# Kernel tuning notes

Measured on AMD Instinct MI355X. Metric: run time of the kernel, lower is better.

## Reference

```python
import jax, jax.numpy as jnp
import numpy as np

B, T, N, D, H = 64, 100, 1000, 128, 8
DK = D // H
TANH_CLIP = 10.0  # standard attention-model logit clipping


def setup_inputs() -> dict:
    key = jax.random.key(0)
    ks = jax.random.split(key, 7)
    embeddings = jax.random.normal(ks[0], (B, N, D), jnp.float32)
    Wkvl = jax.random.normal(ks[1], (D, 3 * D), jnp.float32) * 0.05   # project_node_embeddings
    Wfixed = jax.random.normal(ks[2], (D, D), jnp.float32) * 0.05     # project_fixed_context
    Wctx = jax.random.normal(ks[3], (D, D), jnp.float32) * 0.05       # env context projection
    Wout = jax.random.normal(ks[4], (D, D), jnp.float32) * 0.05       # glimpse output projection
    idx = jax.random.randint(ks[5], (T, B), 0, N, jnp.int32)          # current node per decode step
    action_mask = jax.random.uniform(ks[6], (T, B, N)) > 0.2          # True = feasible
    action_mask = action_mask.at[..., 0].set(True)                    # >=1 feasible action per row
    return {"embeddings": embeddings, "Wkvl": Wkvl, "Wfixed": Wfixed,
            "Wctx": Wctx, "Wout": Wout, "idx": idx, "action_mask": action_mask}


def reference(embeddings, Wkvl, Wfixed, Wctx, Wout, idx, action_mask):
    # ---- _precompute ----
    graph_ctx = embeddings.mean(axis=1) @ Wfixed                      # [B, D]
    gk, gv, lk = jnp.split(embeddings @ Wkvl, 3, axis=-1)             # each [B, N, D]

    # ---- all T decode steps batched (dynamic embeddings are zero / static env) ----
    # NOTE: the source overwrites glimpse_key with glimpse_val (glimpse_key = cached.glimpse_val + dyn)
    # and calls logit_attention(query, glimpse_key, glimpse_key, ...), so keys == values == gv.
    cur = jnp.take_along_axis(embeddings, idx.T[..., None], axis=1)   # [B, T, D] current node embed
    query = graph_ctx[:, None, :] + cur @ Wctx                        # [B, T, D]

    q = query.reshape(B, T, H, DK).transpose(0, 2, 1, 3)              # [B, H, T, dk]
    k = gv.reshape(B, N, H, DK).transpose(0, 2, 1, 3)                 # [B, H, N, dk]
    v = k                                                             # keys == values per source

    infeasible = ~action_mask.transpose(1, 0, 2)                      # [B, T, N]

    # glimpse (inner) attention, masked
    compat = jnp.einsum('bhtd,bhnd->bhtn', q, k) / jnp.sqrt(jnp.float32(DK))
    compat = jnp.where(infeasible[:, None], -jnp.inf, compat)
    attn = jax.nn.softmax(compat, axis=-1)                            # [B, H, T, N]
    glimpse = jnp.einsum('bhtn,bhnd->bthd', attn, v).reshape(B, T, D) @ Wout  # [B, T, D]

    # pointer logits with tanh clipping
    logits = jnp.einsum('btd,bnd->btn', glimpse, lk) / jnp.sqrt(jnp.float32(D))
    logits = TANH_CLIP * jnp.tanh(logits)
    logits = jnp.where(infeasible, -jnp.inf, logits)
    return jax.nn.log_softmax(logits, axis=-1)                        # [B, T, N]
```

## Files before the change

kernel.cpp:

```cpp
#include <hip/hip_runtime.h>
#include <math.h>

#define B_  64
#define T_  100
#define N_  1000
#define NP_ 1024
#define TP_ 112
#define D_  128
#define H_  8
#define DK_ 16

#define NEG_BIG (-1e30f)

#define OFF_GVH  0
#define OFF_LKH  16777216
#define OFF_GVT  33554432
#define OFF_CTX  50331648
#define OFF_QH   50364416
#define OFF_GPH  52199424
#define OFF_WT   53837824
#define OFF_WV   53870592
#define OFF_WCT  53936128
#define OFF_PART 53968896
#define OFF_PM   54231040
#define OFF_OPT  55148544
#define OFF_LP   62488576

typedef __attribute__((ext_vector_type(8))) short short8;
typedef __attribute__((ext_vector_type(4))) short bs4;
typedef __attribute__((ext_vector_type(4))) float f32x4;

#if __has_builtin(__builtin_amdgcn_mfma_f32_16x16x16bf16_1k)
#define MFMA16(a, b, c) __builtin_amdgcn_mfma_f32_16x16x16bf16_1k(a, b, c, 0, 0, 0)
#else
__device__ __forceinline__ f32x4 mfma16_asm(bs4 a, bs4 b, f32x4 c) {
    f32x4 d;
    asm volatile("v_mfma_f32_16x16x16_bf16 %0, %1, %2, %3"
                 : "=v"(d) : "v"(a), "v"(b), "v"(c));
    return d;
}
#define MFMA16(a, b, c) mfma16_asm(a, b, c)
#endif

__device__ __forceinline__ unsigned int f2bf(float f) {
    unsigned int u = __float_as_uint(f);
    return (u + 0x7fffu + ((u >> 16) & 1u)) >> 16;
}
__device__ __forceinline__ unsigned int packbf(float a, float b) {
    return f2bf(a) | (f2bf(b) << 16);
}
__device__ __forceinline__ float bf2f(unsigned short u) {
    return __uint_as_float(((unsigned int)u) << 16);
}

__global__ __launch_bounds__(256) void pre_kernel(
        const float* __restrict__ Wkvl, const float* __restrict__ Wout,
        const float* __restrict__ Wctx, const float* __restrict__ emb,
        const unsigned char* __restrict__ am,
        unsigned short* __restrict__ wv, unsigned short* __restrict__ wt,
        unsigned short* __restrict__ wct, float* __restrict__ part,
        unsigned long long* __restrict__ pm) {
    __shared__ float p2[256];
    int bx = blockIdx.x;
    int tid = threadIdx.x;
    if (bx < 256) {
        int i = bx * 256 + tid;
        if (i < 32768) {
            int n = i >> 7, k = i & 127;
            wv[i] = (unsigned short)f2bf(Wkvl[k * 384 + 128 + n]);
        } else if (i < 49152) {
            int j = i - 32768;
            wt[j] = (unsigned short)f2bf(Wout[(j & 127) * D_ + (j >> 7)]);
        } else {
            int j = i - 49152;
            wct[j] = (unsigned short)f2bf(Wctx[(j & 127) * D_ + (j >> 7)]);
        }
    } else if (bx < 768) {
        int b2 = bx - 256;
        int b = b2 >> 3, c = b2 & 7;
        int d = tid & 127, half = tid >> 7;
        int nstart = c * 125 + (half ? 63 : 0);
        int ncnt = half ? 62 : 63;
        const float* e = emb + ((size_t)b * N_ + nstart) * D_ + d;
        float s = 0.f;
        for (int n = 0; n < ncnt; ++n) s += e[(size_t)n * D_];
        p2[tid] = s;
        __syncthreads();
        if (half == 0) part[((size_t)b * 8 + c) * D_ + d] = p2[d] + p2[d + 128];
    } else {
        int rid = bx - 768;
        int t = rid >> 6;
        int wvx = tid >> 6, lane = tid & 63;
        const unsigned char* amrow = am + (size_t)rid * N_;
        unsigned long long* pmrow = pm + (size_t)rid * 16;
        #pragma unroll
        for (int i = 0; i < 4; ++i) {
            int c = wvx * 4 + i;
            int n = c * 64 + lane;
            unsigned char v = (t < T_ && n < N_) ? amrow[n] : (unsigned char)0;
            unsigned long long mb = __ballot(v != 0);
            if (lane == 0) pmrow[c] = mb;
        }
    }
}

__global__ __launch_bounds__(128) void ctxb_kernel(
        const float* __restrict__ part, const float* __restrict__ Wfixed,
        float* __restrict__ ctx) {
    __shared__ float mean[D_];
    int b = blockIdx.x;
    int d = threadIdx.x;
    float s = 0.f;
    for (int c = 0; c < 8; ++c) s += part[((size_t)b * 8 + c) * D_ + d];
    mean[d] = s * (1.0f / N_);
    __syncthreads();
    float acc = 0.f;
    for (int k = 0; k < D_; ++k) acc += mean[k] * Wfixed[k * D_ + d];
    ctx[b * D_ + d] = acc;
}

__global__ __launch_bounds__(256) void proj_kernel(
        const float* __restrict__ emb, const unsigned short* __restrict__ wv,
        unsigned short* __restrict__ gvh, unsigned short* __restrict__ lkh,
        unsigned short* __restrict__ gvT) {
    __shared__ unsigned short As[64 * 136];
    __shared__ unsigned short Gs[64 * 130];
    int rb = blockIdx.x;
    int tid = threadIdx.x;
    int w = tid >> 6, lane = tid & 63, col = lane & 15, quad = lane >> 4;
    const float* a0 = emb + (size_t)rb * 64 * D_;
    #pragma unroll
    for (int i = 0; i < 8; ++i) {
        int idx = tid + i * 256;
        int r = idx >> 5, kq = idx & 31;
        float4 f = *(const float4*)(a0 + r * D_ + kq * 4);
        *(uint2*)&As[r * 136 + kq * 4] = make_uint2(packbf(f.x, f.y), packbf(f.z, f.w));
    }
    __syncthreads();
    short8 bfr[4][4];
    #pragma unroll
    for (int i = 0; i < 4; ++i) {
        int ncol = i * 64 + w * 16 + col;
        #pragma unroll
        for (int kq = 0; kq < 4; ++kq)
            bfr[i][kq] = *(const short8*)(wv + (size_t)ncol * D_ + kq * 32 + quad * 8);
    }
    #pragma unroll
    for (int mt = 0; mt < 4; ++mt) {
        short8 af[4];
        #pragma unroll
        for (int kq = 0; kq < 4; ++kq)
            af[kq] = *(const short8*)&As[(mt * 16 + col) * 136 + kq * 32 + quad * 8];
        size_t base[4];
        #pragma unroll
        for (int r = 0; r < 4; ++r) {
            int m = rb * 64 + mt * 16 + quad * 4 + r;
            int bb = m / N_;
            int nn = m - bb * N_;
            base[r] = ((size_t)bb * NP_ + nn) * D_;
        }
        #pragma unroll
        for (int i = 0; i < 4; ++i) {
            f32x4 acc = {0.f, 0.f, 0.f, 0.f};
            #pragma unroll
            for (int kq = 0; kq < 4; ++kq)
                acc = __builtin_amdgcn_mfma_f32_16x16x32_bf16(af[kq], bfr[i][kq], acc, 0, 0, 0);
            int ncol = i * 64 + w * 16 + col;
            unsigned short* dst = (ncol < 128) ? gvh : lkh;
            int cc = ncol & 127;
            #pragma unroll
            for (int r = 0; r < 4; ++r) {
                unsigned short hv = (unsigned short)f2bf(acc[r]);
                dst[base[r] + cc] = hv;
                if (ncol < 128)
                    Gs[(mt * 16 + quad * 4 + r) * 130 + ncol] = hv;
            }
        }
    }
    __syncthreads();
    #pragma unroll
    for (int it = 0; it < 32; ++it) {
        int idx = tid + it * 256;
        int d = idx >> 6, nl = idx & 63;
        int m = rb * 64 + nl;
        int bb = m / N_, nn = m - bb * N_;
        gvT[((size_t)bb * D_ + d) * NP_ + nn] = Gs[nl * 130 + d];
    }
}

__global__ __launch_bounds__(256) void query_kernel(
        const float* __restrict__ emb, const unsigned short* __restrict__ wct,
        const float* __restrict__ ctx, const int* __restrict__ idxp,
        unsigned short* __restrict__ qh) {
    __shared__ unsigned short As[64 * 136];
    int blk = blockIdx.x;
    int tid = threadIdx.x;
    int w = tid >> 6, lane = tid & 63, col = lane & 15, quad = lane >> 4;
    #pragma unroll
    for (int i = 0; i < 8; ++i) {
        int idx = tid + i * 256;
        int r = idx >> 5, kq = idx & 31;
        int gr = blk * 64 + r;
        int b = gr / T_, t = gr - b * T_;
        int node = idxp[t * B_ + b];
        float4 f = *(const float4*)(emb + ((size_t)b * N_ + node) * D_ + kq * 4);
        *(uint2*)&As[r * 136 + kq * 4] = make_uint2(packbf(f.x, f.y), packbf(f.z, f.w));
    }
    __syncthreads();
    short8 bfr[2][4];
    #pragma unroll
    for (int i = 0; i < 2; ++i) {
        int ncol = (w * 2 + i) * 16 + col;
        #pragma unroll
        for (int kq = 0; kq < 4; ++kq)
            bfr[i][kq] = *(const short8*)(wct + (size_t)ncol * D_ + kq * 32 + quad * 8);
    }
    #pragma unroll
    for (int mt = 0; mt < 4; ++mt) {
        short8 af[4];
        #pragma unroll
        for (int kq = 0; kq < 4; ++kq)
            af[kq] = *(const short8*)&As[(mt * 16 + col) * 136 + kq * 32 + quad * 8];
        int bb[4], tt_[4];
        #pragma unroll
        for (int r = 0; r < 4; ++r) {
            int gr = blk * 64 + mt * 16 + quad * 4 + r;
            bb[r] = gr / T_; tt_[r] = gr - bb[r] * T_;
        }
        #pragma unroll
        for (int i = 0; i < 2; ++i) {
            f32x4 acc = {0.f, 0.f, 0.f, 0.f};
            #pragma unroll
            for (int kq = 0; kq < 4; ++kq)
                acc = __builtin_amdgcn_mfma_f32_16x16x32_bf16(af[kq], bfr[i][kq], acc, 0, 0, 0);
            int ncol = (w * 2 + i) * 16 + col;
            #pragma unroll
            for (int r = 0; r < 4; ++r) {
                float v = (acc[r] + ctx[bb[r] * D_ + ncol]) * 0.25f;
                qh[((size_t)bb[r] * TP_ + tt_[r]) * D_ + ncol] = (unsigned short)f2bf(v);
            }
        }
    }
}

__global__ __launch_bounds__(512) void attn_part_kernel(
        const unsigned short* __restrict__ gvh, const unsigned short* __restrict__ gvT,
        const unsigned short* __restrict__ qh, const unsigned int* __restrict__ pm32,
        unsigned short* __restrict__ oPartT, float* __restrict__ lPart) {
    int b = blockIdx.x >> 2;
    int slice = blockIdx.x & 3;
    int tid = threadIdx.x;
    int h = tid >> 6, lane = tid & 63;
    int col = lane & 15, quad = lane >> 4;
    int nbase = slice * 256;

    const unsigned short* gvb  = gvh + (size_t)b * NP_ * D_;
    const unsigned short* gvtb = gvT + (size_t)b * D_ * NP_;

    bs4 ka[16], va[16];
    #pragma unroll
    for (int ch = 0; ch < 16; ++ch) {
        int n0 = nbase + ch * 16;
        ka[ch] = *(const bs4*)(gvb + (size_t)(n0 + col) * D_ + h * DK_ + quad * 4);
        va[ch] = *(const bs4*)(gvtb + (size_t)(h * DK_ + col) * NP_ + n0 + quad * 4);
    }

    for (int bt = 0; bt < 7; ++bt) {
        int t0 = bt * 16;
        bs4 qb = *(const bs4*)(qh + ((size_t)b * TP_ + t0 + col) * D_ + h * DK_ + quad * 4);
        const unsigned int* pmrow = pm32 + ((size_t)(t0 + col) * B_ + b) * 32;
        f32x4 oacc = {0.f, 0.f, 0.f, 0.f};
        float lacc = 0.f;
        #pragma unroll
        for (int ch = 0; ch < 16; ++ch) {
            int bitpos = nbase + ch * 16 + quad * 4;
            unsigned int mw = pmrow[bitpos >> 5] >> (bitpos & 31);
            f32x4 z = {0.f, 0.f, 0.f, 0.f};
            f32x4 st = MFMA16(ka[ch], qb, z);
            float e[4];
            #pragma unroll
            for (int r = 0; r < 4; ++r) {
                e[r] = ((mw >> r) & 1u) ? __expf(st[r]) : 0.f;
                lacc += e[r];
            }
            bs4 pb = { (short)f2bf(e[0]), (short)f2bf(e[1]),
                       (short)f2bf(e[2]), (short)f2bf(e[3]) };
            oacc = MFMA16(va[ch], pb, oacc);
        }
        size_t rec = (size_t)(b * 7 + bt) * 4 + slice;
        unsigned short* op = oPartT + rec * 2048;
        float l = lacc;
        l += __shfl_xor(l, 16);
        l += __shfl_xor(l, 32);
        if (lane < 16) lPart[rec * 128 + col * 8 + h] = l;
        #pragma unroll
        for (int r = 0; r < 4; ++r)
            op[(h * DK_ + quad * 4 + r) * 16 + col] = (unsigned short)f2bf(oacc[r]);
    }
}

__global__ __launch_bounds__(256) void attn_comb_kernel(
        const unsigned short* __restrict__ oPartT, const float* __restrict__ lPart,
        const unsigned short* __restrict__ woutT, unsigned short* __restrict__ gph) {
    __shared__ float lsum[16][8];
    __shared__ unsigned short gl[16][144];
    int bx = blockIdx.x;
    int b = bx / 7, bt = bx - b * 7;
    int t0 = bt * 16;
    int tid = threadIdx.x;
    int w = tid >> 6, lane = tid & 63, col = lane & 15, quad = lane >> 4;

    if (tid < 128) {
        int t = tid >> 3, h = tid & 7;
        float l = 0.f;
        #pragma unroll
        for (int s = 0; s < 4; ++s)
            l += lPart[((size_t)bx * 4 + s) * 128 + t * 8 + h];
        lsum[t][h] = l;
    }
    __syncthreads();
    #pragma unroll
    for (int i = 0; i < 8; ++i) {
        int idx = tid + i * 256;
        int d = idx >> 4, t = idx & 15;
        float s = 0.f;
        #pragma unroll
        for (int sl = 0; sl < 4; ++sl)
            s += bf2f(oPartT[((size_t)bx * 4 + sl) * 2048 + idx]);
        gl[t][d] = (unsigned short)f2bf(s / lsum[t][d >> 4]);
    }
    __syncthreads();
    short8 ga[4];
    #pragma unroll
    for (int kq = 0; kq < 4; ++kq)
        ga[kq] = *(const short8*)&gl[col][kq * 32 + quad * 8];
    #pragma unroll
    for (int dt = 0; dt < 2; ++dt) {
        int dob = w * 32 + dt * 16;
        f32x4 od = {0.f, 0.f, 0.f, 0.f};
        #pragma unroll
        for (int kq = 0; kq < 4; ++kq) {
            short8 wb = *(const short8*)(woutT + (size_t)(dob + col) * D_ + kq * 32 + quad * 8);
            od = __builtin_amdgcn_mfma_f32_16x16x32_bf16(ga[kq], wb, od, 0, 0, 0);
        }
        #pragma unroll
        for (int r = 0; r < 4; ++r) {
            int t = t0 + quad * 4 + r;
            if (t < T_)
                gph[((size_t)b * T_ + t) * D_ + dob + col] = (unsigned short)f2bf(od[r]);
        }
    }
}

__global__ __launch_bounds__(256) void logits_kernel(
        const unsigned short* __restrict__ gph, const unsigned short* __restrict__ lkh,
        const unsigned char* __restrict__ am, float* __restrict__ outp) {
    __shared__ unsigned short gs[100 * 136];
    int bx = blockIdx.x;
    int b = bx >> 3, nb = bx & 7;
    int tid = threadIdx.x;
    int w = tid >> 6, lane = tid & 63;
    int col = lane & 15, quad = lane >> 4;

    for (int idx = tid; idx < 3200; idx += 256) {
        int r = idx >> 5, c = idx & 31;
        *(uint2*)&gs[r * 136 + c * 4] =
            *(const uint2*)(gph + ((size_t)b * T_ + r) * D_ + c * 4);
    }
    __syncthreads();

    const unsigned short* lkb = lkh + (size_t)b * NP_ * D_;
    short8 bf[2][4];
    #pragma unroll
    for (int i = 0; i < 2; ++i) {
        int n = nb * 128 + (w * 2 + i) * 16 + col;
        #pragma unroll
        for (int kq = 0; kq < 4; ++kq)
            bf[i][kq] = *(const short8*)(lkb + (size_t)n * D_ + kq * 32 + quad * 8);
    }
    const float rsc = 0.08838834764831845f;
    for (int tt = 0; tt < 7; ++tt) {
        int ta = tt * 16 + col; if (ta > T_ - 1) ta = T_ - 1;
        short8 af[4];
        #pragma unroll
        for (int kq = 0; kq < 4; ++kq)
            af[kq] = *(const short8*)&gs[ta * 136 + kq * 32 + quad * 8];
        #pragma unroll
        for (int i = 0; i < 2; ++i) {
            f32x4 acc = {0.f, 0.f, 0.f, 0.f};
            #pragma unroll
            for (int kq = 0; kq < 4; ++kq)
                acc = __builtin_amdgcn_mfma_f32_16x16x32_bf16(af[kq], bf[i][kq], acc, 0, 0, 0);
            int n = nb * 128 + (w * 2 + i) * 16 + col;
            bool vn = n < N_;
            int nc = vn ? n : (N_ - 1);
            #pragma unroll
            for (int r = 0; r < 4; ++r) {
                int t = tt * 16 + quad * 4 + r;
                if (t < T_ && vn) {
                    bool feas = am[((size_t)t * B_ + b) * N_ + nc] != 0;
                    float y = fminf(fmaxf(2.f * (acc[r] * rsc), -60.f), 60.f);
                    float e = __expf(y);
                    outp[((size_t)b * T_ + t) * N_ + n] =
                        feas ? 10.f * (e - 1.f) / (e + 1.f) : NEG_BIG;
                }
            }
        }
    }
}

__global__ __launch_bounds__(256) void lsm_kernel(float* __restrict__ outp) {
    int row = blockIdx.x * 4 + (threadIdx.x >> 6);
    int lane = threadIdx.x & 63;
    float* p = outp + (size_t)row * N_;
    float v[16];
    float se = 0.f;
    #pragma unroll
    for (int i = 0; i < 16; ++i) {
        int n = lane + i * 64;
        v[i] = (n < N_) ? p[n] : NEG_BIG;
        se += __expf(v[i] - 10.f);
    }
    #pragma unroll
    for (int off = 1; off < 64; off <<= 1) se += __shfl_xor(se, off);
    float lse = 10.f + logf(se);
    #pragma unroll
    for (int i = 0; i < 16; ++i) {
        int n = lane + i * 64;
        if (n < N_) p[n] = v[i] - lse;
    }
}

extern "C" void kernel_launch(void* const* d_in, const int* in_sizes, int n_in,
                              void* d_out, int out_size, void* d_ws, size_t ws_size,
                              hipStream_t stream) {
    const float* emb    = (const float*)d_in[0];
    const float* Wkvl   = (const float*)d_in[1];
    const float* Wfixed = (const float*)d_in[2];
    const float* Wctx   = (const float*)d_in[3];
    const float* Wout   = (const float*)d_in[4];
    const int*   idxp   = (const int*)d_in[5];
    const unsigned char* am = (const unsigned char*)d_in[6];

    char* ws = (char*)d_ws;
    unsigned short* gvh  = (unsigned short*)(ws + OFF_GVH);
    unsigned short* lkh  = (unsigned short*)(ws + OFF_LKH);
    unsigned short* gvT  = (unsigned short*)(ws + OFF_GVT);
    float*          ctx  = (float*)(ws + OFF_CTX);
    unsigned short* qh   = (unsigned short*)(ws + OFF_QH);
    unsigned short* gph  = (unsigned short*)(ws + OFF_GPH);
    unsigned short* wt   = (unsigned short*)(ws + OFF_WT);
    unsigned short* wv   = (unsigned short*)(ws + OFF_WV);
    unsigned short* wct  = (unsigned short*)(ws + OFF_WCT);
    float*          part = (float*)(ws + OFF_PART);
    unsigned long long* pm = (unsigned long long*)(ws + OFF_PM);
    unsigned short* opt  = (unsigned short*)(ws + OFF_OPT);
    float*          lP   = (float*)(ws + OFF_LP);
    float*          outp = (float*)d_out;

    pre_kernel    <<<dim3(7936),  dim3(256), 0, stream>>>(Wkvl, Wout, Wctx, emb, am,
                                                          wv, wt, wct, part, pm);
    ctxb_kernel   <<<dim3(64),    dim3(128), 0, stream>>>(part, Wfixed, ctx);
    proj_kernel   <<<dim3(1000),  dim3(256), 0, stream>>>(emb, wv, gvh, lkh, gvT);
    query_kernel  <<<dim3(100),   dim3(256), 0, stream>>>(emb, wct, ctx, idxp, qh);
    attn_part_kernel<<<dim3(256), dim3(512), 0, stream>>>(gvh, gvT, qh,
                                                          (const unsigned int*)pm, opt, lP);
    attn_comb_kernel<<<dim3(448), dim3(256), 0, stream>>>(opt, lP, wt, gph);
    logits_kernel <<<dim3(512),   dim3(256), 0, stream>>>(gph, lkh, am, outp);
    lsm_kernel    <<<dim3(1600),  dim3(256), 0, stream>>>(outp);
}
```

Baseline: 226.8 us.

## Fuse context, query, attention and combine; fuse logits with log-softmax

Folds the graph-context reduction, query projection, full-N masked attention and output projection into one kernel per (batch, 16-step tile). It drops the split-N partial buffers and the combine pass. Logits are now computed per time tile across all N, and the log-softmax is done in registers, so the output is written once instead of written, read and rewritten. Block-to-batch mapping is arranged by XCD for cache locality. In exchange, each attention block walks all 1000 keys serially, and the context GEMV is recomputed in every block.

Result: slower. 245.0 us (+8.0%).

```diff
diff --git a/kernel.cpp b/kernel.cpp
--- a/kernel.cpp
+++ b/kernel.cpp
@@ -5,7 +5,6 @@
 #define T_  100
 #define N_  1000
 #define NP_ 1024
-#define TP_ 112
 #define D_  128
 #define H_  8
 #define DK_ 16
@@ -15,16 +14,12 @@
 #define OFF_GVH  0
 #define OFF_LKH  16777216
 #define OFF_GVT  33554432
-#define OFF_CTX  50331648
-#define OFF_QH   50364416
 #define OFF_GPH  52199424
 #define OFF_WT   53837824
 #define OFF_WV   53870592
 #define OFF_WCT  53936128
 #define OFF_PART 53968896
 #define OFF_PM   54231040
-#define OFF_OPT  55148544
-#define OFF_LP   62488576
 
 typedef __attribute__((ext_vector_type(8))) short short8;
 typedef __attribute__((ext_vector_type(4))) short bs4;
@@ -104,21 +99,6 @@
     }
 }
 
-__global__ __launch_bounds__(128) void ctxb_kernel(
-        const float* __restrict__ part, const float* __restrict__ Wfixed,
-        float* __restrict__ ctx) {
-    __shared__ float mean[D_];
-    int b = blockIdx.x;
-    int d = threadIdx.x;
-    float s = 0.f;
-    for (int c = 0; c < 8; ++c) s += part[((size_t)b * 8 + c) * D_ + d];
-    mean[d] = s * (1.0f / N_);
-    __syncthreads();
-    float acc = 0.f;
-    for (int k = 0; k < D_; ++k) acc += mean[k] * Wfixed[k * D_ + d];
-    ctx[b * D_ + d] = acc;
-}
-
 __global__ __launch_bounds__(256) void proj_kernel(
         const float* __restrict__ emb, const unsigned short* __restrict__ wv,
         unsigned short* __restrict__ gvh, unsigned short* __restrict__ lkh,
@@ -188,159 +168,123 @@
     }
 }
 
-__global__ __launch_bounds__(256) void query_kernel(
-        const float* __restrict__ emb, const unsigned short* __restrict__ wct,
-        const float* __restrict__ ctx, const int* __restrict__ idxp,
-        unsigned short* __restrict__ qh) {
-    __shared__ unsigned short As[64 * 136];
-    int blk = blockIdx.x;
-    int tid = threadIdx.x;
-    int w = tid >> 6, lane = tid & 63, col = lane & 15, quad = lane >> 4;
-    #pragma unroll
-    for (int i = 0; i < 8; ++i) {
-        int idx = tid + i * 256;
-        int r = idx >> 5, kq = idx & 31;
-        int gr = blk * 64 + r;
-        int b = gr / T_, t = gr - b * T_;
-        int node = idxp[t * B_ + b];
-        float4 f = *(const float4*)(emb + ((size_t)b * N_ + node) * D_ + kq * 4);
-        *(uint2*)&As[r * 136 + kq * 4] = make_uint2(packbf(f.x, f.y), packbf(f.z, f.w));
-    }
-    __syncthreads();
-    short8 bfr[2][4];
-    #pragma unroll
-    for (int i = 0; i < 2; ++i) {
-        int ncol = (w * 2 + i) * 16 + col;
-        #pragma unroll
-        for (int kq = 0; kq < 4; ++kq)
-            bfr[i][kq] = *(const short8*)(wct + (size_t)ncol * D_ + kq * 32 + quad * 8);
-    }
-    #pragma unroll
-    for (int mt = 0; mt < 4; ++mt) {
-        short8 af[4];
-        #pragma unroll
-        for (int kq = 0; kq < 4; ++kq)
-            af[kq] = *(const short8*)&As[(mt * 16 + col) * 136 + kq * 32 + quad * 8];
-        int bb[4], tt_[4];
-        #pragma unroll
-        for (int r = 0; r < 4; ++r) {
-            int gr = blk * 64 + mt * 16 + quad * 4 + r;
-            bb[r] = gr / T_; tt_[r] = gr - bb[r] * T_;
-        }
-        #pragma unroll
-        for (int i = 0; i < 2; ++i) {
-            f32x4 acc = {0.f, 0.f, 0.f, 0.f};
-            #pragma unroll
-            for (int kq = 0; kq < 4; ++kq)
-                acc = __builtin_amdgcn_mfma_f32_16x16x32_bf16(af[kq], bfr[i][kq], acc, 0, 0, 0);
-            int ncol = (w * 2 + i) * 16 + col;
-            #pragma unroll
-            for (int r = 0; r < 4; ++r) {
-                float v = (acc[r] + ctx[bb[r] * D_ + ncol]) * 0.25f;
-                qh[((size_t)bb[r] * TP_ + tt_[r]) * D_ + ncol] = (unsigned short)f2bf(v);
-            }
-        }
-    }
-}
-
-__global__ __launch_bounds__(512) void attn_part_kernel(
+__global__ __launch_bounds__(512) void attn_fused_kernel(
+        const float* __restrict__ emb, const float* __restrict__ Wfixed,
+        const float* __restrict__ part, const unsigned short* __restrict__ wct,
+        const int* __restrict__ idxp,
         const unsigned short* __restrict__ gvh, const unsigned short* __restrict__ gvT,
-        const unsigned short* __restrict__ qh, const unsigned int* __restrict__ pm32,
-        unsigned short* __restrict__ oPartT, float* __restrict__ lPart) {
-    int b = blockIdx.x >> 2;
-    int slice = blockIdx.x & 3;
-    int tid = threadIdx.x;
-    int h = tid >> 6, lane = tid & 63;
-    int col = lane & 15, quad = lane >> 4;
-    int nbase = slice * 256;
-
-    const unsigned short* gvb  = gvh + (size_t)b * NP_ * D_;
-    const unsigned short* gvtb = gvT + (size_t)b * D_ * NP_;
-
-    bs4 ka[16], va[16];
-    #pragma unroll
-    for (int ch = 0; ch < 16; ++ch) {
-        int n0 = nbase + ch * 16;
-        ka[ch] = *(const bs4*)(gvb + (size_t)(n0 + col) * D_ + h * DK_ + quad * 4);
-        va[ch] = *(const bs4*)(gvtb + (size_t)(h * DK_ + col) * NP_ + n0 + quad * 4);
-    }
-
-    for (int bt = 0; bt < 7; ++bt) {
-        int t0 = bt * 16;
-        bs4 qb = *(const bs4*)(qh + ((size_t)b * TP_ + t0 + col) * D_ + h * DK_ + quad * 4);
-        const unsigned int* pmrow = pm32 + ((size_t)(t0 + col) * B_ + b) * 32;
-        f32x4 oacc = {0.f, 0.f, 0.f, 0.f};
-        float lacc = 0.f;
-        #pragma unroll
-        for (int ch = 0; ch < 16; ++ch) {
-            int bitpos = nbase + ch * 16 + quad * 4;
-            unsigned int mw = pmrow[bitpos >> 5] >> (bitpos & 31);
-            f32x4 z = {0.f, 0.f, 0.f, 0.f};
-            f32x4 st = MFMA16(ka[ch], qb, z);
-            float e[4];
-            #pragma unroll
-            for (int r = 0; r < 4; ++r) {
-                e[r] = ((mw >> r) & 1u) ? __expf(st[r]) : 0.f;
-                lacc += e[r];
-            }
-            bs4 pb = { (short)f2bf(e[0]), (short)f2bf(e[1]),
-                       (short)f2bf(e[2]), (short)f2bf(e[3]) };
-            oacc = MFMA16(va[ch], pb, oacc);
-        }
-        size_t rec = (size_t)(b * 7 + bt) * 4 + slice;
-        unsigned short* op = oPartT + rec * 2048;
-        float l = lacc;
-        l += __shfl_xor(l, 16);
-        l += __shfl_xor(l, 32);
-        if (lane < 16) lPart[rec * 128 + col * 8 + h] = l;
-        #pragma unroll
-        for (int r = 0; r < 4; ++r)
-            op[(h * DK_ + quad * 4 + r) * 16 + col] = (unsigned short)f2bf(oacc[r]);
-    }
-}
-
-__global__ __launch_bounds__(256) void attn_comb_kernel(
-        const unsigned short* __restrict__ oPartT, const float* __restrict__ lPart,
-        const unsigned short* __restrict__ woutT, unsigned short* __restrict__ gph) {
-    __shared__ float lsum[16][8];
-    __shared__ unsigned short gl[16][144];
+        const unsigned int* __restrict__ pm32, const unsigned short* __restrict__ wt,
+        unsigned short* __restrict__ gph) {
+    __shared__ float mean_s[D_];
+    __shared__ float cpart[4][D_];
+    __shared__ float ctx_s[D_];
+    __shared__ unsigned short curs[16 * 136];
+    __shared__ unsigned short qs[16 * 136];
+    __shared__ unsigned short gbuf[16 * 136];
+    __shared__ float ls[16][8];
+
     int bx = blockIdx.x;
-    int b = bx / 7, bt = bx - b * 7;
+    int xcd = bx & 7, slot = bx >> 3;
+    int b = (slot / 7) * 8 + xcd;
+    int bt = slot - (slot / 7) * 7;
     int t0 = bt * 16;
     int tid = threadIdx.x;
     int w = tid >> 6, lane = tid & 63, col = lane & 15, quad = lane >> 4;
-
-    if (tid < 128) {
-        int t = tid >> 3, h = tid & 7;
-        float l = 0.f;
-        #pragma unroll
-        for (int s = 0; s < 4; ++s)
-            l += lPart[((size_t)bx * 4 + s) * 128 + t * 8 + h];
-        lsum[t][h] = l;
-    }
-    __syncthreads();
-    #pragma unroll
-    for (int i = 0; i < 8; ++i) {
-        int idx = tid + i * 256;
-        int d = idx >> 4, t = idx & 15;
+    int h = w;
+
+    {
+        int r = tid >> 5, c = tid & 31;
+        int t = t0 + r; if (t > T_ - 1) t = T_ - 1;
+        int node = idxp[t * B_ + b];
+        float4 f = *(const float4*)(emb + ((size_t)b * N_ + node) * D_ + c * 4);
+        *(uint2*)&curs[r * 136 + c * 4] = make_uint2(packbf(f.x, f.y), packbf(f.z, f.w));
+    }
+    if (tid < D_) {
         float s = 0.f;
         #pragma unroll
-        for (int sl = 0; sl < 4; ++sl)
-            s += bf2f(oPartT[((size_t)bx * 4 + sl) * 2048 + idx]);
-        gl[t][d] = (unsigned short)f2bf(s / lsum[t][d >> 4]);
-    }
-    __syncthreads();
-    short8 ga[4];
-    #pragma unroll
-    for (int kq = 0; kq < 4; ++kq)
-        ga[kq] = *(const short8*)&gl[col][kq * 32 + quad * 8];
-    #pragma unroll
-    for (int dt = 0; dt < 2; ++dt) {
-        int dob = w * 32 + dt * 16;
+        for (int c = 0; c < 8; ++c) s += part[((size_t)b * 8 + c) * D_ + tid];
+        mean_s[tid] = s * (1.0f / N_);
+    }
+    __syncthreads();
+    {
+        int d = tid & 127, kh = tid >> 7;
+        float acc = 0.f;
+        #pragma unroll
+        for (int k = 0; k < 32; ++k)
+            acc += mean_s[kh * 32 + k] * Wfixed[(size_t)(kh * 32 + k) * D_ + d];
+        cpart[kh][d] = acc;
+    }
+    __syncthreads();
+    if (tid < D_)
+        ctx_s[tid] = cpart[0][tid] + cpart[1][tid] + cpart[2][tid] + cpart[3][tid];
+    __syncthreads();
+
+    {
+        short8 af[4], bfr[4];
+        #pragma unroll
+        for (int kq = 0; kq < 4; ++kq) {
+            af[kq]  = *(const short8*)&curs[col * 136 + kq * 32 + quad * 8];
+            bfr[kq] = *(const short8*)(wct + (size_t)(w * 16 + col) * D_ + kq * 32 + quad * 8);
+        }
+        f32x4 acc = {0.f, 0.f, 0.f, 0.f};
+        #pragma unroll
+        for (int kq = 0; kq < 4; ++kq)
+            acc = __builtin_amdgcn_mfma_f32_16x16x32_bf16(af[kq], bfr[kq], acc, 0, 0, 0);
+        #pragma unroll
+        for (int r = 0; r < 4; ++r) {
+            float v = (acc[r] + ctx_s[w * 16 + col]) * 0.25f;
+            qs[(quad * 4 + r) * 136 + w * 16 + col] = (unsigned short)f2bf(v);
+        }
+    }
+    __syncthreads();
+
+    const unsigned short* gvb  = gvh + (size_t)b * NP_ * D_;
+    const unsigned short* gvtb = gvT + (size_t)b * D_ * NP_;
+    bs4 qb = *(const bs4*)&qs[col * 136 + h * DK_ + quad * 4];
+    const unsigned int* pmrow = pm32 + ((size_t)(t0 + col) * B_ + b) * 32;
+
+    f32x4 oacc = {0.f, 0.f, 0.f, 0.f};
+    float lacc = 0.f;
+    #pragma unroll 8
+    for (int ch = 0; ch < 64; ++ch) {
+        int n0 = ch * 16;
+        bs4 ka = *(const bs4*)(gvb + (size_t)(n0 + col) * D_ + h * DK_ + quad * 4);
+        bs4 va = *(const bs4*)(gvtb + (size_t)(h * DK_ + col) * NP_ + n0 + quad * 4);
+        int bitpos = n0 + quad * 4;
+        unsigned int mw = pmrow[bitpos >> 5] >> (bitpos & 31);
+        f32x4 z = {0.f, 0.f, 0.f, 0.f};
+        f32x4 st = MFMA16(ka, qb, z);
+        float e[4];
+        #pragma unroll
+        for (int r = 0; r < 4; ++r) {
+            e[r] = ((mw >> r) & 1u) ? __expf(st[r]) : 0.f;
+            lacc += e[r];
+        }
+        bs4 pb = { (short)f2bf(e[0]), (short)f2bf(e[1]),
+                   (short)f2bf(e[2]), (short)f2bf(e[3]) };
+        oacc = MFMA16(va, pb, oacc);
+    }
+    lacc += __shfl_xor(lacc, 16);
+    lacc += __shfl_xor(lacc, 32);
+    if (lane < 16) ls[col][h] = lacc;
+    __syncthreads();
+    {
+        float inv = 1.0f / ls[col][h];
+        #pragma unroll
+        for (int r = 0; r < 4; ++r)
+            gbuf[col * 136 + h * DK_ + quad * 4 + r] = (unsigned short)f2bf(oacc[r] * inv);
+    }
+    __syncthreads();
+    {
+        short8 ga[4];
+        #pragma unroll
+        for (int kq = 0; kq < 4; ++kq)
+            ga[kq] = *(const short8*)&gbuf[col * 136 + kq * 32 + quad * 8];
+        int dob = w * 16;
         f32x4 od = {0.f, 0.f, 0.f, 0.f};
         #pragma unroll
         for (int kq = 0; kq < 4; ++kq) {
-            short8 wb = *(const short8*)(woutT + (size_t)(dob + col) * D_ + kq * 32 + quad * 8);
+            short8 wb = *(const short8*)(wt + (size_t)(dob + col) * D_ + kq * 32 + quad * 8);
             od = __builtin_amdgcn_mfma_f32_16x16x32_bf16(ga[kq], wb, od, 0, 0, 0);
         }
         #pragma unroll
@@ -352,82 +296,90 @@
     }
 }
 
-__global__ __launch_bounds__(256) void logits_kernel(
+__global__ __launch_bounds__(512) void logits_lsm_kernel(
         const unsigned short* __restrict__ gph, const unsigned short* __restrict__ lkh,
         const unsigned char* __restrict__ am, float* __restrict__ outp) {
-    __shared__ unsigned short gs[100 * 136];
+    __shared__ unsigned short gs[16 * 136];
+    __shared__ float lsP[8][17];
     int bx = blockIdx.x;
-    int b = bx >> 3, nb = bx & 7;
+    int xcd = bx & 7, slot = bx >> 3;
+    int b = (slot / 7) * 8 + xcd;
+    int bt = slot - (slot / 7) * 7;
+    int t0 = bt * 16;
     int tid = threadIdx.x;
-    int w = tid >> 6, lane = tid & 63;
-    int col = lane & 15, quad = lane >> 4;
-
-    for (int idx = tid; idx < 3200; idx += 256) {
-        int r = idx >> 5, c = idx & 31;
+    int w = tid >> 6, lane = tid & 63, col = lane & 15, quad = lane >> 4;
+
+    {
+        int r = tid >> 5, c = tid & 31;
+        int t = t0 + r; if (t > T_ - 1) t = T_ - 1;
         *(uint2*)&gs[r * 136 + c * 4] =
-            *(const uint2*)(gph + ((size_t)b * T_ + r) * D_ + c * 4);
-    }
-    __syncthreads();
+            *(const uint2*)(gph + ((size_t)b * T_ + t) * D_ + c * 4);
+    }
+    __syncthreads();
+
+    short8 af[4];
+    #pragma unroll
+    for (int kq = 0; kq < 4; ++kq)
+        af[kq] = *(const short8*)&gs[col * 136 + kq * 32 + quad * 8];
 
     const unsigned short* lkb = lkh + (size_t)b * NP_ * D_;
-    short8 bf[2][4];
-    #pragma unroll
-    for (int i = 0; i < 2; ++i) {
-        int n = nb * 128 + (w * 2 + i) * 16 + col;
-        #pragma unroll
-        for (int kq = 0; kq < 4; ++kq)
-            bf[i][kq] = *(const short8*)(lkb + (size_t)n * D_ + kq * 32 + quad * 8);
-    }
     const float rsc = 0.08838834764831845f;
-    for (int tt = 0; tt < 7; ++tt) {
-        int ta = tt * 16 + col; if (ta > T_ - 1) ta = T_ - 1;
-        short8 af[4];
-        #pragma unroll
-        for (int kq = 0; kq < 4; ++kq)
-            af[kq] = *(const short8*)&gs[ta * 136 + kq * 32 + quad * 8];
-        #pragma unroll
-        for (int i = 0; i < 2; ++i) {
-            f32x4 acc = {0.f, 0.f, 0.f, 0.f};
-            #pragma unroll
-            for (int kq = 0; kq < 4; ++kq)
-                acc = __builtin_amdgcn_mfma_f32_16x16x32_bf16(af[kq], bf[i][kq], acc, 0, 0, 0);
-            int n = nb * 128 + (w * 2 + i) * 16 + col;
-            bool vn = n < N_;
-            int nc = vn ? n : (N_ - 1);
+    float y[8][4];
+    float es[4] = {0.f, 0.f, 0.f, 0.f};
+    #pragma unroll
+    for (int i = 0; i < 8; ++i) {
+        int n = w * 128 + i * 16 + col;
+        f32x4 acc = {0.f, 0.f, 0.f, 0.f};
+        #pragma unroll
+        for (int kq = 0; kq < 4; ++kq) {
+            short8 bf = *(const short8*)(lkb + (size_t)n * D_ + kq * 32 + quad * 8);
+            acc = __builtin_amdgcn_mfma_f32_16x16x32_bf16(af[kq], bf, acc, 0, 0, 0);
+        }
+        bool vn = n < N_;
+        #pragma unroll
+        for (int r = 0; r < 4; ++r) {
+            int t = t0 + quad * 4 + r;
+            float yv = fminf(fmaxf(2.f * (acc[r] * rsc), -60.f), 60.f);
+            float ex = __expf(yv);
+            float th = 10.f * (ex - 1.f) / (ex + 1.f);
+            bool feas = (t < T_) && vn &&
+                        (am[((size_t)t * B_ + b) * N_ + (vn ? n : 0)] != 0);
+            y[i][r] = feas ? th : NEG_BIG;
+            es[r] += feas ? __expf(th - 10.f) : 0.f;
+        }
+    }
+    #pragma unroll
+    for (int r = 0; r < 4; ++r) {
+        float s = es[r];
+        s += __shfl_xor(s, 1); s += __shfl_xor(s, 2);
+        s += __shfl_xor(s, 4); s += __shfl_xor(s, 8);
+        es[r] = s;
+    }
+    if (col == 0) {
+        #pragma unroll
+        for (int r = 0; r < 4; ++r) lsP[w][quad * 4 + r] = es[r];
+    }
+    __syncthreads();
+    float lse[4];
+    #pragma unroll
+    for (int r = 0; r < 4; ++r) {
+        int tl = quad * 4 + r;
+        float s = 0.f;
+        #pragma unroll
+        for (int ww = 0; ww < 8; ++ww) s += lsP[ww][tl];
+        lse[r] = 10.f + logf(s);
+    }
+    #pragma unroll
+    for (int i = 0; i < 8; ++i) {
+        int n = w * 128 + i * 16 + col;
+        if (n < N_) {
             #pragma unroll
             for (int r = 0; r < 4; ++r) {
-                int t = tt * 16 + quad * 4 + r;
-                if (t < T_ && vn) {
-                    bool feas = am[((size_t)t * B_ + b) * N_ + nc] != 0;
-                    float y = fminf(fmaxf(2.f * (acc[r] * rsc), -60.f), 60.f);
-                    float e = __expf(y);
-                    outp[((size_t)b * T_ + t) * N_ + n] =
-                        feas ? 10.f * (e - 1.f) / (e + 1.f) : NEG_BIG;
-                }
+                int t = t0 + quad * 4 + r;
+                if (t < T_)
+                    outp[((size_t)b * T_ + t) * N_ + n] = y[i][r] - lse[r];
             }
         }
-    }
-}
-
-__global__ __launch_bounds__(256) void lsm_kernel(float* __restrict__ outp) {
-    int row = blockIdx.x * 4 + (threadIdx.x >> 6);
-    int lane = threadIdx.x & 63;
-    float* p = outp + (size_t)row * N_;
-    float v[16];
-    float se = 0.f;
-    #pragma unroll
-    for (int i = 0; i < 16; ++i) {
-        int n = lane + i * 64;
-        v[i] = (n < N_) ? p[n] : NEG_BIG;
-        se += __expf(v[i] - 10.f);
-    }
-    #pragma unroll
-    for (int off = 1; off < 64; off <<= 1) se += __shfl_xor(se, off);
-    float lse = 10.f + logf(se);
-    #pragma unroll
-    for (int i = 0; i < 16; ++i) {
-        int n = lane + i * 64;
-        if (n < N_) p[n] = v[i] - lse;
     }
 }
 
@@ -446,26 +398,19 @@
     unsigned short* gvh  = (unsigned short*)(ws + OFF_GVH);
     unsigned short* lkh  = (unsigned short*)(ws + OFF_LKH);
     unsigned short* gvT  = (unsigned short*)(ws + OFF_GVT);
-    float*          ctx  = (float*)(ws + OFF_CTX);
-    unsigned short* qh   = (unsigned short*)(ws + OFF_QH);
     unsigned short* gph  = (unsigned short*)(ws + OFF_GPH);
     unsigned short* wt   = (unsigned short*)(ws + OFF_WT);
     unsigned short* wv   = (unsigned short*)(ws + OFF_WV);
     unsigned short* wct  = (unsigned short*)(ws + OFF_WCT);
     float*          part = (float*)(ws + OFF_PART);
     unsigned long long* pm = (unsigned long long*)(ws + OFF_PM);
-    unsigned short* opt  = (unsigned short*)(ws + OFF_OPT);
-    float*          lP   = (float*)(ws + OFF_LP);
     float*          outp = (float*)d_out;
 
-    pre_kernel    <<<dim3(7936),  dim3(256), 0, stream>>>(Wkvl, Wout, Wctx, emb, am,
-                                                          wv, wt, wct, part, pm);
-    ctxb_kernel   <<<dim3(64),    dim3(128), 0, stream>>>(part, Wfixed, ctx);
-    proj_kernel   <<<dim3(1000),  dim3(256), 0, stream>>>(emb, wv, gvh, lkh, gvT);
-    query_kernel  <<<dim3(100),   dim3(256), 0, stream>>>(emb, wct, ctx, idxp, qh);
-    attn_part_kernel<<<dim3(256), dim3(512), 0, stream>>>(gvh, gvT, qh,
-                                                          (const unsigned int*)pm, opt, lP);
-    attn_comb_kernel<<<dim3(448), dim3(256), 0, stream>>>(opt, lP, wt, gph);
-    logits_kernel <<<dim3(512),   dim3(256), 0, stream>>>(gph, lkh, am, outp);
-    lsm_kernel    <<<dim3(1600),  dim3(256), 0, stream>>>(outp);
-}
+    pre_kernel      <<<dim3(7936), dim3(256), 0, stream>>>(Wkvl, Wout, Wctx, emb, am,
+                                                           wv, wt, wct, part, pm);
+    proj_kernel     <<<dim3(1000), dim3(256), 0, stream>>>(emb, wv, gvh, lkh, gvT);
+    attn_fused_kernel<<<dim3(448), dim3(512), 0, stream>>>(emb, Wfixed, part, wct, idxp,
+                                                           gvh, gvT, (const unsigned int*)pm,
+                                                           wt, gph);
+    logits_lsm_kernel<<<dim3(448), dim3(512), 0, stream>>>(gph, lkh, am, outp);
+}
```

## Fuse pointer-logit GEMM with log-softmax in one kernel per row tile

Applied to the files above, without the earlier changes.

Replaces the separate logits and log-softmax kernels with one kernel. Each block of 512 threads owns 16 decode steps across all 1024 nodes of one batch. Logits stay in registers, row sums come from shuffles plus a small shared buffer, and the final log-probabilities are written once. This removes a full write, read and rewrite pass over the 25.6M-float output. In exchange, every block reloads its lk tile from global memory (lk reuse across time tiles is lost), each thread holds more registers, and blocks are mapped to batches with an XCD-aware index.

Result: faster. 220.0 us (-3.0%).

```diff
diff --git a/kernel.cpp b/kernel.cpp
--- a/kernel.cpp
+++ b/kernel.cpp
@@ -352,82 +352,90 @@
     }
 }
 
-__global__ __launch_bounds__(256) void logits_kernel(
+__global__ __launch_bounds__(512) void logits_lsm_kernel(
         const unsigned short* __restrict__ gph, const unsigned short* __restrict__ lkh,
         const unsigned char* __restrict__ am, float* __restrict__ outp) {
-    __shared__ unsigned short gs[100 * 136];
+    __shared__ unsigned short gs[16 * 136];
+    __shared__ float lsP[8][17];
     int bx = blockIdx.x;
-    int b = bx >> 3, nb = bx & 7;
-    int tid = threadIdx.x;
-    int w = tid >> 6, lane = tid & 63;
-    int col = lane & 15, quad = lane >> 4;
-
-    for (int idx = tid; idx < 3200; idx += 256) {
-        int r = idx >> 5, c = idx & 31;
+    int xcd = bx & 7, slot = bx >> 3;
+    int b = (slot / 7) * 8 + xcd;
+    int bt = slot - (slot / 7) * 7;
+    int t0 = bt * 16;
+    int tid = threadIdx.x;
+    int w = tid >> 6, lane = tid & 63, col = lane & 15, quad = lane >> 4;
+
+    {
+        int r = tid >> 5, c = tid & 31;
+        int t = t0 + r; if (t > T_ - 1) t = T_ - 1;
         *(uint2*)&gs[r * 136 + c * 4] =
-            *(const uint2*)(gph + ((size_t)b * T_ + r) * D_ + c * 4);
-    }
-    __syncthreads();
+            *(const uint2*)(gph + ((size_t)b * T_ + t) * D_ + c * 4);
+    }
+    __syncthreads();
+
+    short8 af[4];
+    #pragma unroll
+    for (int kq = 0; kq < 4; ++kq)
+        af[kq] = *(const short8*)&gs[col * 136 + kq * 32 + quad * 8];
 
     const unsigned short* lkb = lkh + (size_t)b * NP_ * D_;
-    short8 bf[2][4];
-    #pragma unroll
-    for (int i = 0; i < 2; ++i) {
-        int n = nb * 128 + (w * 2 + i) * 16 + col;
-        #pragma unroll
-        for (int kq = 0; kq < 4; ++kq)
-            bf[i][kq] = *(const short8*)(lkb + (size_t)n * D_ + kq * 32 + quad * 8);
-    }
     const float rsc = 0.08838834764831845f;
-    for (int tt = 0; tt < 7; ++tt) {
-        int ta = tt * 16 + col; if (ta > T_ - 1) ta = T_ - 1;
-        short8 af[4];
-        #pragma unroll
-        for (int kq = 0; kq < 4; ++kq)
-            af[kq] = *(const short8*)&gs[ta * 136 + kq * 32 + quad * 8];
-        #pragma unroll
-        for (int i = 0; i < 2; ++i) {
-            f32x4 acc = {0.f, 0.f, 0.f, 0.f};
-            #pragma unroll
-            for (int kq = 0; kq < 4; ++kq)
-                acc = __builtin_amdgcn_mfma_f32_16x16x32_bf16(af[kq], bf[i][kq], acc, 0, 0, 0);
-            int n = nb * 128 + (w * 2 + i) * 16 + col;
-            bool vn = n < N_;
-            int nc = vn ? n : (N_ - 1);
+    float y[8][4];
+    float es[4] = {0.f, 0.f, 0.f, 0.f};
+    #pragma unroll
+    for (int i = 0; i < 8; ++i) {
+        int n = w * 128 + i * 16 + col;
+        f32x4 acc = {0.f, 0.f, 0.f, 0.f};
+        #pragma unroll
+        for (int kq = 0; kq < 4; ++kq) {
+            short8 bf = *(const short8*)(lkb + (size_t)n * D_ + kq * 32 + quad * 8);
+            acc = __builtin_amdgcn_mfma_f32_16x16x32_bf16(af[kq], bf, acc, 0, 0, 0);
+        }
+        bool vn = n < N_;
+        #pragma unroll
+        for (int r = 0; r < 4; ++r) {
+            int t = t0 + quad * 4 + r;
+            float yv = fminf(fmaxf(2.f * (acc[r] * rsc), -60.f), 60.f);
+            float ex = __expf(yv);
+            float th = 10.f * (ex - 1.f) / (ex + 1.f);
+            bool feas = (t < T_) && vn &&
+                        (am[((size_t)t * B_ + b) * N_ + (vn ? n : 0)] != 0);
+            y[i][r] = feas ? th : NEG_BIG;
+            es[r] += feas ? __expf(th - 10.f) : 0.f;
+        }
+    }
+    #pragma unroll
+    for (int r = 0; r < 4; ++r) {
+        float s = es[r];
+        s += __shfl_xor(s, 1); s += __shfl_xor(s, 2);
+        s += __shfl_xor(s, 4); s += __shfl_xor(s, 8);
+        es[r] = s;
+    }
+    if (col == 0) {
+        #pragma unroll
+        for (int r = 0; r < 4; ++r) lsP[w][quad * 4 + r] = es[r];
+    }
+    __syncthreads();
+    float lse[4];
+    #pragma unroll
+    for (int r = 0; r < 4; ++r) {
+        int tl = quad * 4 + r;
+        float s = 0.f;
+        #pragma unroll
+        for (int ww = 0; ww < 8; ++ww) s += lsP[ww][tl];
+        lse[r] = 10.f + logf(s);
+    }
+    #pragma unroll
+    for (int i = 0; i < 8; ++i) {
+        int n = w * 128 + i * 16 + col;
+        if (n < N_) {
             #pragma unroll
             for (int r = 0; r < 4; ++r) {
-                int t = tt * 16 + quad * 4 + r;
-                if (t < T_ && vn) {
-                    bool feas = am[((size_t)t * B_ + b) * N_ + nc] != 0;
-                    float y = fminf(fmaxf(2.f * (acc[r] * rsc), -60.f), 60.f);
-                    float e = __expf(y);
-                    outp[((size_t)b * T_ + t) * N_ + n] =
-                        feas ? 10.f * (e - 1.f) / (e + 1.f) : NEG_BIG;
-                }
+                int t = t0 + quad * 4 + r;
+                if (t < T_)
+                    outp[((size_t)b * T_ + t) * N_ + n] = y[i][r] - lse[r];
             }
         }
-    }
-}
-
-__global__ __launch_bounds__(256) void lsm_kernel(float* __restrict__ outp) {
-    int row = blockIdx.x * 4 + (threadIdx.x >> 6);
-    int lane = threadIdx.x & 63;
-    float* p = outp + (size_t)row * N_;
-    float v[16];
-    float se = 0.f;
-    #pragma unroll
-    for (int i = 0; i < 16; ++i) {
-        int n = lane + i * 64;
-        v[i] = (n < N_) ? p[n] : NEG_BIG;
-        se += __expf(v[i] - 10.f);
-    }
-    #pragma unroll
-    for (int off = 1; off < 64; off <<= 1) se += __shfl_xor(se, off);
-    float lse = 10.f + logf(se);
-    #pragma unroll
-    for (int i = 0; i < 16; ++i) {
-        int n = lane + i * 64;
-        if (n < N_) p[n] = v[i] - lse;
     }
 }
 
@@ -458,14 +466,13 @@
     float*          lP   = (float*)(ws + OFF_LP);
     float*          outp = (float*)d_out;
 
-    pre_kernel    <<<dim3(7936),  dim3(256), 0, stream>>>(Wkvl, Wout, Wctx, emb, am,
-                                                          wv, wt, wct, part, pm);
-    ctxb_kernel   <<<dim3(64),    dim3(128), 0, stream>>>(part, Wfixed, ctx);
-    proj_kernel   <<<dim3(1000),  dim3(256), 0, stream>>>(emb, wv, gvh, lkh, gvT);
-    query_kernel  <<<dim3(100),   dim3(256), 0, stream>>>(emb, wct, ctx, idxp, qh);
-    attn_part_kernel<<<dim3(256), dim3(512), 0, stream>>>(gvh, gvT, qh,
-                                                          (const unsigned int*)pm, opt, lP);
-    attn_comb_kernel<<<dim3(448), dim3(256), 0, stream>>>(opt, lP, wt, gph);
-    logits_kernel <<<dim3(512),   dim3(256), 0, stream>>>(gph, lkh, am, outp);
-    lsm_kernel    <<<dim3(1600),  dim3(256), 0, stream>>>(outp);
-}
+    pre_kernel      <<<dim3(7936), dim3(256), 0, stream>>>(Wkvl, Wout, Wctx, emb, am,
+                                                           wv, wt, wct, part, pm);
+    ctxb_kernel     <<<dim3(64),   dim3(128), 0, stream>>>(part, Wfixed, ctx);
+    proj_kernel     <<<dim3(1000), dim3(256), 0, stream>>>(emb, wv, gvh, lkh, gvT);
+    query_kernel    <<<dim3(100),  dim3(256), 0, stream>>>(emb, wct, ctx, idxp, qh);
+    attn_part_kernel<<<dim3(256),  dim3(512), 0, stream>>>(gvh, gvT, qh,
+                                                           (const unsigned int*)pm, opt, lP);
+    attn_comb_kernel<<<dim3(448),  dim3(256), 0, stream>>>(opt, lP, wt, gph);
+    logits_lsm_kernel<<<dim3(448), dim3(512), 0, stream>>>(gph, lkh, am, outp);
+}
```
